# Kernel optimization log

Measured on AMD Instinct MI355X. Metric: run time of the kernel, lower is better.

The kernel has to match this reference:

```python
import jax, jax.numpy as jnp
import numpy as np

VOCAB, EMBED, HIDDEN, NCLS = 50257, 64, 64, 5
B, S = 4096, 512
BN_EPS = 1e-5


def setup_inputs() -> dict:
    key = jax.random.key(0)
    ks = jax.random.split(key, 10)
    x = jax.random.randint(ks[0], (B, S), 0, VOCAB, dtype=jnp.int64 if jax.config.jax_enable_x64 else jnp.int32)
    emb = jax.random.normal(ks[1], (VOCAB, EMBED), dtype=jnp.float32)
    emb = emb.at[0].set(0.0)  # padding_idx=0
    s = 1.0 / np.sqrt(HIDDEN)
    W_ih = jax.random.uniform(ks[2], (HIDDEN, EMBED), minval=-s, maxval=s, dtype=jnp.float32)
    W_hh = jax.random.uniform(ks[3], (HIDDEN, HIDDEN), minval=-s, maxval=s, dtype=jnp.float32)
    b_ih = jax.random.uniform(ks[4], (HIDDEN,), minval=-s, maxval=s, dtype=jnp.float32)
    b_hh = jax.random.uniform(ks[5], (HIDDEN,), minval=-s, maxval=s, dtype=jnp.float32)
    gamma = jnp.ones((HIDDEN,), dtype=jnp.float32)
    beta = jnp.zeros((HIDDEN,), dtype=jnp.float32)
    sf = 1.0 / np.sqrt(HIDDEN)
    W_fc = jax.random.uniform(ks[6], (NCLS, HIDDEN), minval=-sf, maxval=sf, dtype=jnp.float32)
    b_fc = jax.random.uniform(ks[7], (NCLS,), minval=-sf, maxval=sf, dtype=jnp.float32)
    return {"x": x, "emb": emb, "W_ih": W_ih, "W_hh": W_hh, "b_ih": b_ih,
            "b_hh": b_hh, "gamma": gamma, "beta": beta, "W_fc": W_fc, "b_fc": b_fc}


def reference(x, emb, W_ih, W_hh, b_ih, b_hh, gamma, beta, W_fc, b_fc):
    # embedding gather: [B, S, E]
    xe = emb[x]
    # precompute input projection once: [B, S, H] -> scan over time as [S, B, H]
    xp = jnp.einsum('bse,he->bsh', xe, W_ih) + b_ih + b_hh
    xp_t = jnp.swapaxes(xp, 0, 1)

    def step(h, xt):
        h = jnp.tanh(xt + h @ W_hh.T)
        return h, None

    h0 = jnp.zeros((x.shape[0], HIDDEN), dtype=xp.dtype)
    h_n, _ = jax.lax.scan(step, h0, xp_t)

    # BatchNorm1d (training-mode math: batch stats, biased variance)
    mean = jnp.mean(h_n, axis=0)
    var = jnp.mean((h_n - mean) ** 2, axis=0)
    h_bn = (h_n - mean) * jax.lax.rsqrt(var + BN_EPS) * gamma + beta
    # dropout is identity in eval / deterministic reference
    logits = h_bn @ W_fc.T + b_fc  # [B, 5]
    return logits
```

## Files before the change

### kernel.cpp

```cpp
#include <hip/hip_runtime.h>

typedef _Float16 f16;
typedef __attribute__((ext_vector_type(4))) _Float16 f16x4;
typedef __attribute__((ext_vector_type(8))) _Float16 f16x8;
typedef __attribute__((ext_vector_type(4))) float f32x4;

constexpr int BATCH  = 4096;
constexpr int SEQ    = 512;
constexpr int HID    = 64;
constexpr int VOCAB  = 50257;
constexpr int NBLK_GEMM = 786;
constexpr float LOG2E2 = 2.8853900817779268f;

#define MFMA_K32(a, b, c) __builtin_amdgcn_mfma_f32_16x16x32_f16(a, b, c, 0, 0, 0)

__global__ __launch_bounds__(256) void prep_kernel(
    const float* __restrict__ emb, const float* __restrict__ Wih,
    const float* __restrict__ Whh, const float* __restrict__ bih,
    const float* __restrict__ bhh,
    f16* __restrict__ embP, f16* __restrict__ whh_f, float* __restrict__ bn_acc)
{
  const int bid = blockIdx.x;
  const int tid = threadIdx.x;
  if (bid == NBLK_GEMM) {
    #pragma unroll
    for (int k = 0; k < 16; ++k) {
      const int i = tid * 16 + k;
      whh_f[i] = (f16)(Whh[i] * LOG2E2);
    }
    if (tid < 128) bn_acc[tid] = 0.f;
    return;
  }
  const int w = tid >> 6;
  const int L = tid & 63;
  const int n = L & 15;
  const int q = L >> 4;
  const int R0 = (bid * 4 + w) * 16;
  int v = R0 + n;
  const bool ok = v < VOCAB;
  if (!ok) v = VOCAB - 1;

  f16x8 Wi[4][2];
  f32x4 bias[4];
  #pragma unroll
  for (int f = 0; f < 4; ++f) {
    const float* wr = Wih + (16 * f + n) * 64;
    #pragma unroll
    for (int h = 0; h < 2; ++h) {
      float4 w0 = *(const float4*)(wr + 32 * h + 8 * q);
      float4 w1 = *(const float4*)(wr + 32 * h + 8 * q + 4);
      Wi[f][h] = (f16x8){
        (f16)(w0.x * LOG2E2), (f16)(w0.y * LOG2E2),
        (f16)(w0.z * LOG2E2), (f16)(w0.w * LOG2E2),
        (f16)(w1.x * LOG2E2), (f16)(w1.y * LOG2E2),
        (f16)(w1.z * LOG2E2), (f16)(w1.w * LOG2E2)};
    }
    float4 bi = *(const float4*)(bih + 16 * f + 4 * q);
    float4 bh = *(const float4*)(bhh + 16 * f + 4 * q);
    bias[f] = (f32x4){(bi.x + bh.x) * LOG2E2, (bi.y + bh.y) * LOG2E2,
                      (bi.z + bh.z) * LOG2E2, (bi.w + bh.w) * LOG2E2};
  }

  const float* er = emb + (long)v * 64;
  float4 a0 = *(const float4*)(er + 8 * q);
  float4 a1 = *(const float4*)(er + 8 * q + 4);
  float4 a2 = *(const float4*)(er + 32 + 8 * q);
  float4 a3 = *(const float4*)(er + 32 + 8 * q + 4);
  f16x8 e0 = (f16x8){(f16)a0.x, (f16)a0.y, (f16)a0.z, (f16)a0.w,
                     (f16)a1.x, (f16)a1.y, (f16)a1.z, (f16)a1.w};
  f16x8 e1 = (f16x8){(f16)a2.x, (f16)a2.y, (f16)a2.z, (f16)a2.w,
                     (f16)a3.x, (f16)a3.y, (f16)a3.z, (f16)a3.w};

  f32x4 D[4];
  #pragma unroll
  for (int f = 0; f < 4; ++f) {
    D[f] = MFMA_K32(Wi[f][0], e0, bias[f]);
    D[f] = MFMA_K32(Wi[f][1], e1, D[f]);
  }
  if (ok) {
    f16* orow = embP + (long)v * 64 + 4 * q;
    #pragma unroll
    for (int f = 0; f < 4; ++f) {
      f16x4 o = (f16x4){(f16)D[f][0], (f16)D[f][1], (f16)D[f][2], (f16)D[f][3]};
      *(f16x4*)(orow + 16 * f) = o;
    }
  }
}

__global__ __launch_bounds__(64, 1) void rnn_scan_kernel(
    const int* __restrict__ xx, const f16* __restrict__ embP,
    const f16* __restrict__ whh,
    float* __restrict__ hT , float* __restrict__ bn_acc)
{
  const int L = threadIdx.x;
  const int n = L & 15;
  const int q = L >> 4;
  const int R0 = blockIdx.x << 4;

  f16x8 Wp[4][2];
  #pragma unroll
  for (int f = 0; f < 4; ++f) {
    const f16* wr = whh + (16 * f + n) * 64;
    #pragma unroll
    for (int c = 0; c < 2; ++c) {
      f16x4 lo = *(const f16x4*)(wr + 32 * c + 4 * q);
      f16x4 hi = *(const f16x4*)(wr + 32 * c + 16 + 4 * q);
      Wp[f][c] = __builtin_shufflevector(lo, hi, 0, 4, 1, 5, 2, 6, 3, 7);
    }
  }

  f16x8 hB01 = {0, 0, 0, 0, 0, 0, 0, 0};
  f16x8 hB23 = {0, 0, 0, 0, 0, 0, 0, 0};

  const int4* x4 = (const int4*)(xx + (R0 + n) * SEQ);
  int4 K1 = x4[1];

  const f16* ebase = embP + 4 * q;
  f16x4 g[4][4];
  {
    int4 K0 = x4[0];
    const int id0[4] = {K0.x, K0.y, K0.z, K0.w};
    #pragma unroll
    for (int u = 0; u < 4; ++u) {
      const f16* eb = ebase + (long)id0[u] * 64;
      #pragma unroll
      for (int f = 0; f < 4; ++f) g[u][f] = *(const f16x4*)(eb + 16 * f);
    }
  }

  for (int t = 0; t < SEQ / 4; ++t) {
    int4 K2 = x4[(t + 2 < SEQ / 4) ? t + 2 : SEQ / 4 - 1];
    const int nid[4] = {K1.x, K1.y, K1.z, K1.w};
    const bool lastt = (t == SEQ / 4 - 1);

    #pragma unroll
    for (int u = 0; u < 4; ++u) {
      f32x4 D0 = (f32x4){(float)g[u][0][0], (float)g[u][0][1],
                         (float)g[u][0][2], (float)g[u][0][3]};
      f32x4 D1 = (f32x4){(float)g[u][1][0], (float)g[u][1][1],
                         (float)g[u][1][2], (float)g[u][1][3]};
      f32x4 D2 = (f32x4){(float)g[u][2][0], (float)g[u][2][1],
                         (float)g[u][2][2], (float)g[u][2][3]};
      f32x4 D3 = (f32x4){(float)g[u][3][0], (float)g[u][3][1],
                         (float)g[u][3][2], (float)g[u][3][3]};

      D0 = MFMA_K32(Wp[0][0], hB01, D0);
      D1 = MFMA_K32(Wp[1][0], hB01, D1);
      D2 = MFMA_K32(Wp[2][0], hB01, D2);
      D3 = MFMA_K32(Wp[3][0], hB01, D3);

      {
        const f16* eb = ebase + (long)nid[u] * 64;
        #pragma unroll
        for (int f = 0; f < 4; ++f) g[u][f] = *(const f16x4*)(eb + 16 * f);
      }

      D0 = MFMA_K32(Wp[0][1], hB23, D0);
      D1 = MFMA_K32(Wp[1][1], hB23, D1);
      D2 = MFMA_K32(Wp[2][1], hB23, D2);
      D3 = MFMA_K32(Wp[3][1], hB23, D3);

      float th[4][4];
      #pragma unroll
      for (int r = 0; r < 4; ++r) {
        float x0 = __builtin_amdgcn_exp2f(D0[r]);
        float x1 = __builtin_amdgcn_exp2f(D1[r]);
        float x2 = __builtin_amdgcn_exp2f(D2[r]);
        float x3 = __builtin_amdgcn_exp2f(D3[r]);
        th[0][r] = fmaf(-2.0f, __builtin_amdgcn_rcpf(x0 + 1.0f), 1.0f);
        th[1][r] = fmaf(-2.0f, __builtin_amdgcn_rcpf(x1 + 1.0f), 1.0f);
        th[2][r] = fmaf(-2.0f, __builtin_amdgcn_rcpf(x2 + 1.0f), 1.0f);
        th[3][r] = fmaf(-2.0f, __builtin_amdgcn_rcpf(x3 + 1.0f), 1.0f);
        hB01[2 * r]     = (f16)th[0][r];
        hB01[2 * r + 1] = (f16)th[1][r];
        hB23[2 * r]     = (f16)th[2][r];
        hB23[2 * r + 1] = (f16)th[3][r];
      }

      if (lastt && u == 3) {
        #pragma unroll
        for (int f = 0; f < 4; ++f) {
          #pragma unroll
          for (int r = 0; r < 4; ++r) {
            float v = th[f][r];
            const int feat = 16 * f + 4 * q + r;
            hT[feat * BATCH + R0 + n] = v;
            float s1 = v, s2 = v * v;
            s1 += __shfl_xor(s1, 1, 64);  s2 += __shfl_xor(s2, 1, 64);
            s1 += __shfl_xor(s1, 2, 64);  s2 += __shfl_xor(s2, 2, 64);
            s1 += __shfl_xor(s1, 4, 64);  s2 += __shfl_xor(s2, 4, 64);
            s1 += __shfl_xor(s1, 8, 64);  s2 += __shfl_xor(s2, 8, 64);
            if (n == 0) {
              atomicAdd(bn_acc + feat, s1);
              atomicAdd(bn_acc + 64 + feat, s2);
            }
          }
        }
      }
    }
    K1 = K2;
  }
}

__global__ __launch_bounds__(256) void head_kernel(
    const float* __restrict__ hT, const float* __restrict__ bn_acc,
    const float* __restrict__ gamma, const float* __restrict__ beta,
    const float* __restrict__ Wfc, const float* __restrict__ bfc,
    float* __restrict__ out)
{
  __shared__ float sc[64], sh[64];
  const int tid = threadIdx.x;
  if (tid < 64) {
    float mean = bn_acc[tid] * (1.0f / BATCH);
    float var  = bn_acc[64 + tid] * (1.0f / BATCH) - mean * mean;
    float inv  = rsqrtf(var + 1e-5f);
    float s    = gamma[tid] * inv;
    sc[tid] = s;
    sh[tid] = beta[tid] - mean * s;
  }
  __syncthreads();
  const int b = blockIdx.x * 256 + tid;
  float acc[5];
  #pragma unroll
  for (int c = 0; c < 5; ++c) acc[c] = bfc[c];
  for (int j = 0; j < HID; ++j) {
    float hv  = hT[j * BATCH + b];
    float hat = fmaf(hv, sc[j], sh[j]);
    #pragma unroll
    for (int c = 0; c < 5; ++c) acc[c] = fmaf(hat, Wfc[c * 64 + j], acc[c]);
  }
  #pragma unroll
  for (int c = 0; c < 5; ++c) out[b * 5 + c] = acc[c];
}

extern "C" void kernel_launch(void* const* d_in, const int* in_sizes, int n_in,
                              void* d_out, int out_size, void* d_ws, size_t ws_size,
                              hipStream_t stream)
{
  const int*   x     = (const int*)d_in[0];
  const float* emb   = (const float*)d_in[1];
  const float* W_ih  = (const float*)d_in[2];
  const float* W_hh  = (const float*)d_in[3];
  const float* b_ih  = (const float*)d_in[4];
  const float* b_hh  = (const float*)d_in[5];
  const float* gamma = (const float*)d_in[6];
  const float* beta  = (const float*)d_in[7];
  const float* W_fc  = (const float*)d_in[8];
  const float* b_fc  = (const float*)d_in[9];

  char* ws = (char*)d_ws;
  float* hT     = (float*)ws;
  float* bn_acc = (float*)(ws + 1048576);
  f16*   embP   = (f16*)(ws + 1049088);
  f16*   whh_f  = (f16*)(ws + 7481984);

  prep_kernel<<<dim3(NBLK_GEMM + 1), dim3(256), 0, stream>>>(
      emb, W_ih, W_hh, b_ih, b_hh, embP, whh_f, bn_acc);
  rnn_scan_kernel<<<dim3(BATCH / 16), dim3(64), 0, stream>>>(
      x, embP, whh_f, hT, bn_acc);
  head_kernel<<<dim3(BATCH / 256), dim3(256), 0, stream>>>(
      hT, bn_acc, gamma, beta, W_fc, b_fc, (float*)d_out);
}
```

Baseline: 297.3 us.

## Split RNN hidden features across two waves with LDS exchange per step

After: 265.9 us. 10.6% less time.

```diff
diff --git a/kernel.cpp b/kernel.cpp
--- a/kernel.cpp
+++ b/kernel.cpp
@@ -87,46 +87,51 @@
   }
 }
 
-__global__ __launch_bounds__(64, 1) void rnn_scan_kernel(
+__global__ __launch_bounds__(128, 1) void rnn_scan_kernel(
     const int* __restrict__ xx, const f16* __restrict__ embP,
     const f16* __restrict__ whh,
     float* __restrict__ hT , float* __restrict__ bn_acc)
 {
-  const int L = threadIdx.x;
+  __shared__ int4 xslot[2][2][64];
+  const int tid = threadIdx.x;
+  const int w = tid >> 6;
+  const int L = tid & 63;
   const int n = L & 15;
   const int q = L >> 4;
   const int R0 = blockIdx.x << 4;
 
-  f16x8 Wp[4][2];
-  #pragma unroll
-  for (int f = 0; f < 4; ++f) {
-    const f16* wr = whh + (16 * f + n) * 64;
+  f16x8 Wp[2][2];
+  #pragma unroll
+  for (int j = 0; j < 2; ++j) {
+    const f16* wr = whh + (16 * (2 * w + j) + n) * 64;
     #pragma unroll
     for (int c = 0; c < 2; ++c) {
       f16x4 lo = *(const f16x4*)(wr + 32 * c + 4 * q);
       f16x4 hi = *(const f16x4*)(wr + 32 * c + 16 + 4 * q);
-      Wp[f][c] = __builtin_shufflevector(lo, hi, 0, 4, 1, 5, 2, 6, 3, 7);
-    }
-  }
-
-  f16x8 hB01 = {0, 0, 0, 0, 0, 0, 0, 0};
-  f16x8 hB23 = {0, 0, 0, 0, 0, 0, 0, 0};
+      Wp[j][c] = __builtin_shufflevector(lo, hi, 0, 4, 1, 5, 2, 6, 3, 7);
+    }
+  }
+
+  f16x8 hOwn = {0, 0, 0, 0, 0, 0, 0, 0};
+  xslot[0][w][L] = int4{0, 0, 0, 0};
 
   const int4* x4 = (const int4*)(xx + (R0 + n) * SEQ);
   int4 K1 = x4[1];
 
-  const f16* ebase = embP + 4 * q;
-  f16x4 g[4][4];
+  const f16* ebase = embP + 32 * w + 4 * q;
+  f16x4 g0[4], g1[4];
   {
     int4 K0 = x4[0];
     const int id0[4] = {K0.x, K0.y, K0.z, K0.w};
     #pragma unroll
     for (int u = 0; u < 4; ++u) {
       const f16* eb = ebase + (long)id0[u] * 64;
-      #pragma unroll
-      for (int f = 0; f < 4; ++f) g[u][f] = *(const f16x4*)(eb + 16 * f);
-    }
-  }
+      g0[u] = *(const f16x4*)(eb);
+      g1[u] = *(const f16x4*)(eb + 16);
+    }
+  }
+
+  asm volatile("s_waitcnt lgkmcnt(0)\n\ts_barrier" ::: "memory");
 
   for (int t = 0; t < SEQ / 4; ++t) {
     int4 K2 = x4[(t + 2 < SEQ / 4) ? t + 2 : SEQ / 4 - 1];
@@ -135,55 +140,74 @@
 
     #pragma unroll
     for (int u = 0; u < 4; ++u) {
-      f32x4 D0 = (f32x4){(float)g[u][0][0], (float)g[u][0][1],
-                         (float)g[u][0][2], (float)g[u][0][3]};
-      f32x4 D1 = (f32x4){(float)g[u][1][0], (float)g[u][1][1],
-                         (float)g[u][1][2], (float)g[u][1][3]};
-      f32x4 D2 = (f32x4){(float)g[u][2][0], (float)g[u][2][1],
-                         (float)g[u][2][2], (float)g[u][2][3]};
-      f32x4 D3 = (f32x4){(float)g[u][3][0], (float)g[u][3][1],
-                         (float)g[u][3][2], (float)g[u][3][3]};
-
-      D0 = MFMA_K32(Wp[0][0], hB01, D0);
-      D1 = MFMA_K32(Wp[1][0], hB01, D1);
-      D2 = MFMA_K32(Wp[2][0], hB01, D2);
-      D3 = MFMA_K32(Wp[3][0], hB01, D3);
+      const int p = u & 1;
+      int4 oraw = xslot[p][w ^ 1][L];
+
+      f32x4 D0 = (f32x4){(float)g0[u][0], (float)g0[u][1],
+                         (float)g0[u][2], (float)g0[u][3]};
+      f32x4 D1 = (f32x4){(float)g1[u][0], (float)g1[u][1],
+                         (float)g1[u][2], (float)g1[u][3]};
+
+      D0 = MFMA_K32(Wp[0][w], hOwn, D0);
+      D1 = MFMA_K32(Wp[1][w], hOwn, D1);
 
       {
         const f16* eb = ebase + (long)nid[u] * 64;
-        #pragma unroll
-        for (int f = 0; f < 4; ++f) g[u][f] = *(const f16x4*)(eb + 16 * f);
-      }
-
-      D0 = MFMA_K32(Wp[0][1], hB23, D0);
-      D1 = MFMA_K32(Wp[1][1], hB23, D1);
-      D2 = MFMA_K32(Wp[2][1], hB23, D2);
-      D3 = MFMA_K32(Wp[3][1], hB23, D3);
-
-      float th[4][4];
+        g0[u] = *(const f16x4*)(eb);
+        g1[u] = *(const f16x4*)(eb + 16);
+      }
+
+      union { int4 i; f16x8 h; } cv; cv.i = oraw;
+      D0 = MFMA_K32(Wp[0][w ^ 1], cv.h, D0);
+      D1 = MFMA_K32(Wp[1][w ^ 1], cv.h, D1);
+
+      float A0[4], A1[4];
       #pragma unroll
       for (int r = 0; r < 4; ++r) {
-        float x0 = __builtin_amdgcn_exp2f(D0[r]);
-        float x1 = __builtin_amdgcn_exp2f(D1[r]);
-        float x2 = __builtin_amdgcn_exp2f(D2[r]);
-        float x3 = __builtin_amdgcn_exp2f(D3[r]);
-        th[0][r] = fmaf(-2.0f, __builtin_amdgcn_rcpf(x0 + 1.0f), 1.0f);
-        th[1][r] = fmaf(-2.0f, __builtin_amdgcn_rcpf(x1 + 1.0f), 1.0f);
-        th[2][r] = fmaf(-2.0f, __builtin_amdgcn_rcpf(x2 + 1.0f), 1.0f);
-        th[3][r] = fmaf(-2.0f, __builtin_amdgcn_rcpf(x3 + 1.0f), 1.0f);
-        hB01[2 * r]     = (f16)th[0][r];
-        hB01[2 * r + 1] = (f16)th[1][r];
-        hB23[2 * r]     = (f16)th[2][r];
-        hB23[2 * r + 1] = (f16)th[3][r];
-      }
+        A0[r] = __builtin_amdgcn_exp2f(fminf(D0[r], 16.0f)) + 1.0f;
+        A1[r] = __builtin_amdgcn_exp2f(fminf(D1[r], 16.0f)) + 1.0f;
+      }
+      float th0[4], th1[4];
+      {
+        float t1 = A0[0] * A0[1], t2 = t1 * A0[2], t3 = t2 * A0[3];
+        float rr = __builtin_amdgcn_rcpf(t3);
+        float i3 = rr * t2;
+        float s3 = rr * A0[3];
+        float i2 = s3 * t1;
+        float s2 = s3 * A0[2];
+        th0[0] = fmaf(-2.0f, s2 * A0[1], 1.0f);
+        th0[1] = fmaf(-2.0f, s2 * A0[0], 1.0f);
+        th0[2] = fmaf(-2.0f, i2, 1.0f);
+        th0[3] = fmaf(-2.0f, i3, 1.0f);
+      }
+      {
+        float t1 = A1[0] * A1[1], t2 = t1 * A1[2], t3 = t2 * A1[3];
+        float rr = __builtin_amdgcn_rcpf(t3);
+        float i3 = rr * t2;
+        float s3 = rr * A1[3];
+        float i2 = s3 * t1;
+        float s2 = s3 * A1[2];
+        th1[0] = fmaf(-2.0f, s2 * A1[1], 1.0f);
+        th1[1] = fmaf(-2.0f, s2 * A1[0], 1.0f);
+        th1[2] = fmaf(-2.0f, i2, 1.0f);
+        th1[3] = fmaf(-2.0f, i3, 1.0f);
+      }
+      #pragma unroll
+      for (int r = 0; r < 4; ++r) {
+        hOwn[2 * r]     = (f16)th0[r];
+        hOwn[2 * r + 1] = (f16)th1[r];
+      }
+
+      union { f16x8 h; int4 i; } cw; cw.h = hOwn;
+      xslot[p ^ 1][w][L] = cw.i;
 
       if (lastt && u == 3) {
         #pragma unroll
-        for (int f = 0; f < 4; ++f) {
+        for (int j = 0; j < 2; ++j) {
           #pragma unroll
           for (int r = 0; r < 4; ++r) {
-            float v = th[f][r];
-            const int feat = 16 * f + 4 * q + r;
+            float v = j ? th1[r] : th0[r];
+            const int feat = 16 * (2 * w + j) + 4 * q + r;
             hT[feat * BATCH + R0 + n] = v;
             float s1 = v, s2 = v * v;
             s1 += __shfl_xor(s1, 1, 64);  s2 += __shfl_xor(s2, 1, 64);
@@ -197,6 +221,8 @@
           }
         }
       }
+
+      asm volatile("s_waitcnt lgkmcnt(0)\n\ts_barrier" ::: "memory");
     }
     K1 = K2;
   }
@@ -256,7 +282,7 @@
 
   prep_kernel<<<dim3(NBLK_GEMM + 1), dim3(256), 0, stream>>>(
       emb, W_ih, W_hh, b_ih, b_hh, embP, whh_f, bn_acc);
-  rnn_scan_kernel<<<dim3(BATCH / 16), dim3(64), 0, stream>>>(
+  rnn_scan_kernel<<<dim3(BATCH / 16), dim3(128), 0, stream>>>(
       x, embP, whh_f, hT, bn_acc);
   head_kernel<<<dim3(BATCH / 256), dim3(256), 0, stream>>>(
       hT, bn_acc, gamma, beta, W_fc, b_fc, (float*)d_out);
```
